# Kernel tuning notes

Measured on AMD Instinct MI355X. Metric: run time of the kernel, lower is better.

## Reference

```python
import jax, jax.numpy as jnp
import numpy as np
import math

B, S, D_MODEL = 8, 1024, 1024
N_INPUT, N_PROCESS = 256, 512
N_HEADS, N_HEADS_IN = 8, 4
HIDDEN = 2 * N_INPUT  # combination_analyzer hidden dim (default n_input*2)
TEMP = 2.0            # router temperature buffer


def _mha(x, w_in, b_in, w_out, b_out, n_heads):
    """torch nn.MultiheadAttention (batch_first, eval mode) self-attention."""
    Bq, Sq, E = x.shape
    qkv = x @ w_in.T + b_in                      # [B,S,3E]
    q, k, v = jnp.split(qkv, 3, axis=-1)
    dh = E // n_heads
    sh = lambda t: t.reshape(Bq, Sq, n_heads, dh).transpose(0, 2, 1, 3)
    q, k, v = sh(q), sh(k), sh(v)
    scores = jnp.einsum('bhqd,bhkd->bhqk', q, k) * (1.0 / math.sqrt(dh))
    attn = jax.nn.softmax(scores, axis=-1)
    out = jnp.einsum('bhqk,bhkd->bhqd', attn, v).transpose(0, 2, 1, 3).reshape(Bq, Sq, E)
    return out @ w_out.T + b_out


def _ln(x, g, b, eps=1e-5):
    m = x.mean(-1, keepdims=True)
    v = ((x - m) ** 2).mean(-1, keepdims=True)
    return (x - m) / jnp.sqrt(v + eps) * g + b


def setup_inputs() -> dict:
    key = jax.random.key(0)
    ks = jax.random.split(key, 24)
    rn = lambda i, shape, s=0.02: jax.random.normal(ks[i], shape, jnp.float32) * s
    return {
        'x': jax.random.normal(ks[0], (B, S, D_MODEL), jnp.float32),
        # DynamicRouter attention (embed=d_model, heads=8)
        'r_in_w': rn(1, (3 * D_MODEL, D_MODEL)), 'r_in_b': jnp.zeros((3 * D_MODEL,), jnp.float32),
        'r_out_w': rn(2, (D_MODEL, D_MODEL)), 'r_out_b': jnp.zeros((D_MODEL,), jnp.float32),
        'aff_w': rn(3, (N_INPUT, D_MODEL)), 'aff_b': jnp.zeros((N_INPUT,), jnp.float32),
        # InputNeurons
        'patterns': rn(4, (N_INPUT, D_MODEL), 0.05),
        'i_in_w': rn(5, (3 * N_INPUT, N_INPUT)), 'i_in_b': jnp.zeros((3 * N_INPUT,), jnp.float32),
        'i_out_w': rn(6, (N_INPUT, N_INPUT)), 'i_out_b': jnp.zeros((N_INPUT,), jnp.float32),
        'ln_g': jnp.ones((N_INPUT,), jnp.float32), 'ln_b': jnp.zeros((N_INPUT,), jnp.float32),
        # ProcessNeurons
        'comb_w': rn(7, (N_PROCESS, N_INPUT), 0.05),
        'out_proj_w': rn(8, (N_PROCESS, D_MODEL), 0.05),
        'a1_w': rn(9, (HIDDEN, N_INPUT)), 'a1_b': jnp.zeros((HIDDEN,), jnp.float32),
        'a2_w': rn(10, (N_PROCESS, HIDDEN)), 'a2_b': jnp.zeros((N_PROCESS,), jnp.float32),
        'k_input': 128, 'k_process': 256,
    }


def reference(x, r_in_w, r_in_b, r_out_w, r_out_b, aff_w, aff_b, patterns,
              i_in_w, i_in_b, i_out_w, i_out_b, ln_g, ln_b,
              comb_w, out_proj_w, a1_w, a1_b, a2_w, a2_b, k_input, k_process):
    Bq = x.shape[0]
    # ---- DynamicRouter (eval mode: no gumbel noise, no score noise) ----
    context = _mha(x, r_in_w, r_in_b, r_out_w, r_out_b, N_HEADS)      # [B,S,D]
    affinity = context @ aff_w.T + aff_b                              # [B,S,N_INPUT]
    scores = affinity.max(axis=1)                                     # [B,N_INPUT]
    logits = scores / TEMP
    soft_w = jax.nn.softmax(logits, axis=-1)
    _, indices = jax.lax.top_k(logits, k_input)                       # [B,k_in]
    mask = jnp.zeros_like(soft_w).at[jnp.arange(Bq)[:, None], indices].set(1.0)
    masked = soft_w * mask
    weights = masked / (masked.sum(-1, keepdims=True) + 1e-8)         # [B,N_INPUT]
    # ---- InputNeurons (eval: dropout off) ----
    acts = jax.nn.gelu(context @ patterns.T, approximate=False)       # [B,S,N_INPUT]
    attn_out = _mha(acts, i_in_w, i_in_b, i_out_w, i_out_b, N_HEADS_IN)
    acts = _ln(acts + attn_out, ln_g, ln_b)
    # ---- Gather routed input neurons, weighted by routing weights ----
    sel_acts = jnp.take_along_axis(acts, indices[:, None, :], axis=2)  # [B,S,k_in]
    sel_w = jnp.take_along_axis(weights, indices, axis=1)              # [B,k_in]
    sel_acts = sel_acts * sel_w[:, None, :]
    # ---- ProcessNeurons ----
    # selected_weights[b,p,j] = comb_w[p, indices[b,j]]
    sel_cw = jnp.take(comb_w, indices, axis=1).transpose(1, 0, 2)      # [B,P,k_in]
    proc_acts = jax.nn.gelu(jnp.einsum('bsk,bpk->bsp', sel_acts, sel_cw), approximate=False)
    input_sel = jnp.zeros((Bq, N_INPUT), jnp.float32).at[jnp.arange(Bq)[:, None], indices].set(1.0)
    relevance = jax.nn.gelu(input_sel @ a1_w.T + a1_b, approximate=False) @ a2_w.T + a2_b  # [B,P]
    act_scores = proc_acts.max(axis=1)                                 # [B,P]
    final_scores = act_scores * jax.nn.sigmoid(relevance)
    _, pidx = jax.lax.top_k(final_scores, k_process)                   # [B,k_p]
    sel_proc = jnp.take_along_axis(proc_acts, pidx[:, None, :], axis=2)  # [B,S,k_p]
    sel_proj = out_proj_w[pidx]                                        # [B,k_p,D]
    out = jnp.einsum('bsk,bkd->bsd', sel_proc, sel_proj)               # [B,S,D]
    # ---- residual (eval: dropout identity) ----
    return x + out
```

## Files before the change

kernel.cpp:

```cpp
#include <hip/hip_runtime.h>
#include <hip/hip_bf16.h>
#include <math.h>

constexpr int NB = 8, NS = 1024, ND = 1024, NIN = 256, NPROC = 512, KIN = 128, KPROC = 256;

typedef __attribute__((ext_vector_type(8))) short bf16x8;
typedef __attribute__((ext_vector_type(4))) float f32x4;

#define VMCNT(n) asm volatile("s_waitcnt vmcnt(" #n ")" ::: "memory")
#define LGKMCNT(n) asm volatile("s_waitcnt lgkmcnt(" #n ")" ::: "memory")

__device__ inline float gelu_f(float x) {
    return 0.5f * x * (1.0f + erff(x * 0.7071067811865476f));
}
__device__ inline unsigned short f2b(float f) {
    __hip_bfloat16 h = __float2bfloat16(f);
    return *reinterpret_cast<unsigned short*>(&h);
}
__device__ inline float b2f(unsigned short u) {
    unsigned int v = (unsigned int)u << 16;
    return __uint_as_float(v);
}
__device__ inline void gload16(const void* g, void* l) {
    __builtin_amdgcn_global_load_lds(
        (const __attribute__((address_space(1))) void*)g,
        (__attribute__((address_space(3))) void*)l, 16, 0, 0);
}

__global__ __launch_bounds__(256)
void cvt_all_kernel(const float* __restrict__ x, const float* __restrict__ rin,
                    const float* __restrict__ rout, const float* __restrict__ affw,
                    const float* __restrict__ patt, const float* __restrict__ iin,
                    const float* __restrict__ iout, const float* __restrict__ aff_b,
                    unsigned short* __restrict__ xb, unsigned short* __restrict__ rinb,
                    unsigned short* __restrict__ routb, unsigned short* __restrict__ affbw,
                    unsigned short* __restrict__ pattb, unsigned short* __restrict__ iinb,
                    unsigned short* __restrict__ ioutb, float* __restrict__ biascat)
{
    if (blockIdx.x == 0) {
        int t = threadIdx.x;
        biascat[t] = aff_b[t];
        biascat[256 + t] = 0.f;
    }
    long gi = (long)blockIdx.x * 256 + threadIdx.x;
    long stride = (long)gridDim.x * 256;
    for (; gi < 3342336; gi += stride) {
        const float4* s; ushort4* d; long off;
        if (gi < 2097152)      { s = (const float4*)x;    d = (ushort4*)xb;    off = gi; }
        else if (gi < 2883584) { s = (const float4*)rin;  d = (ushort4*)rinb;  off = gi - 2097152; }
        else if (gi < 3145728) { s = (const float4*)rout; d = (ushort4*)routb; off = gi - 2883584; }
        else if (gi < 3211264) { s = (const float4*)affw; d = (ushort4*)affbw; off = gi - 3145728; }
        else if (gi < 3276800) { s = (const float4*)patt; d = (ushort4*)pattb; off = gi - 3211264; }
        else if (gi < 3325952) { s = (const float4*)iin;  d = (ushort4*)iinb;  off = gi - 3276800; }
        else                   { s = (const float4*)iout; d = (ushort4*)ioutb; off = gi - 3325952; }
        float4 v = s[off];
        ushort4 o;
        o.x = f2b(v.x); o.y = f2b(v.y); o.z = f2b(v.z); o.w = f2b(v.w);
        d[off] = o;
    }
}

__global__ __launch_bounds__(256)
void gemm128s(const unsigned short* __restrict__ A, int lda,
              const unsigned short* __restrict__ B, int ldb,
              const float* __restrict__ bias,
              unsigned short* __restrict__ C16, int ldc,
              int K, int nbx)
{
    __shared__ __align__(16) unsigned short Ab[3][128 * 32];
    __shared__ __align__(16) unsigned short Bb[3][128 * 32];
    int o = blockIdx.x;
    int cpx = gridDim.x >> 3;
    int swz = (o & 7) * cpx + (o >> 3);
    int by = swz / nbx, bx = swz - by * nbx;
    int row0 = by * 128, col0 = bx * 128;

    int t = threadIdx.x;
    int w = t >> 6, l = t & 63, l15 = l & 15, g = l >> 4;
    int wr = w >> 1, wc = w & 1;
    int NT = K >> 5;

    f32x4 acc[4][4];
#pragma unroll
    for (int i = 0; i < 4; ++i)
#pragma unroll
        for (int j = 0; j < 4; ++j) acc[i][j] = (f32x4){0.f, 0.f, 0.f, 0.f};

    auto STAGE = [&](int c, int kt) {
        int k0 = kt * 32;
#pragma unroll
        for (int i = 0; i < 2; ++i) {
            int gi = t + i * 256;
            int row = gi >> 2, cg = gi & 3;
            int cgs = cg ^ ((row >> 1) & 3);
            gload16(&A[(long)(row0 + row) * lda + k0 + cgs * 8], &Ab[c][gi * 8]);
        }
#pragma unroll
        for (int i = 0; i < 2; ++i) {
            int gi = t + i * 256;
            int row = gi >> 2, cg = gi & 3;
            int cgs = cg ^ ((row >> 1) & 3);
            gload16(&B[(long)(col0 + row) * ldb + k0 + cgs * 8], &Bb[c][gi * 8]);
        }
    };

    STAGE(0, 0);
    STAGE(1, 1);

    int cbr = (g ^ ((l15 >> 1) & 3)) * 16;

    int cur = 0;
    for (int T = 0; T < NT; ++T) {
        if (T + 1 < NT) { VMCNT(4); } else { VMCNT(0); }
        __builtin_amdgcn_s_barrier();
        asm volatile("" ::: "memory");

        const char* Ab_ = (const char*)&Ab[cur][0];
        const char* Bb_ = (const char*)&Bb[cur][0];
        bf16x8 af[4], bfr[4];
#pragma unroll
        for (int mi = 0; mi < 4; ++mi)
            af[mi] = *(const bf16x8*)(Ab_ + (wr * 64 + mi * 16 + l15) * 64 + cbr);
#pragma unroll
        for (int ni = 0; ni < 4; ++ni)
            bfr[ni] = *(const bf16x8*)(Bb_ + (wc * 64 + ni * 16 + l15) * 64 + cbr);

        if (T + 2 < NT) {
            int nxt = cur + 2;
            if (nxt >= 3) nxt -= 3;
            STAGE(nxt, T + 2);
        }

        LGKMCNT(0);
        __builtin_amdgcn_sched_barrier(0);
        __builtin_amdgcn_s_setprio(1);
#pragma unroll
        for (int mi = 0; mi < 4; ++mi)
#pragma unroll
            for (int ni = 0; ni < 4; ++ni)
                acc[mi][ni] = __builtin_amdgcn_mfma_f32_16x16x32_bf16(
                    af[mi], bfr[ni], acc[mi][ni], 0, 0, 0);
        __builtin_amdgcn_s_setprio(0);

        cur = (cur == 2) ? 0 : cur + 1;
    }

#pragma unroll
    for (int mi = 0; mi < 4; ++mi) {
#pragma unroll
        for (int ni = 0; ni < 4; ++ni) {
            int col = col0 + wc * 64 + ni * 16 + l15;
            float bv = bias ? bias[col] : 0.f;
#pragma unroll
            for (int r = 0; r < 4; ++r) {
                int row = row0 + wr * 64 + mi * 16 + g * 4 + r;
                float v = acc[mi][ni][r] + bv;
                float vp = __shfl_xor(v, 1);
                if (!(l15 & 1)) {
                    unsigned int u = (unsigned int)f2b(v) | ((unsigned int)f2b(vp) << 16);
                    *(unsigned int*)&C16[(long)row * ldc + col] = u;
                }
            }
        }
    }
}

__global__ __launch_bounds__(256)
void gemm128x64(const unsigned short* __restrict__ A, int lda,
                const unsigned short* __restrict__ B, int ldb,
                const float* __restrict__ bias,
                unsigned short* __restrict__ C16, int ldc,
                int K, int nbx)
{
    __shared__ __align__(16) unsigned short Ab[3][128 * 32];
    __shared__ __align__(16) unsigned short Bb[3][64 * 32];
    int o = blockIdx.x;
    int cpx = gridDim.x >> 3;
    int swz = (o & 7) * cpx + (o >> 3);
    int by = swz / nbx, bx = swz - by * nbx;
    int row0 = by * 128, col0 = bx * 64;

    int t = threadIdx.x;
    int w = t >> 6, l = t & 63, l15 = l & 15, g = l >> 4;
    int wr = w >> 1, wc = w & 1;
    int NT = K >> 5;

    f32x4 acc[4][2];
#pragma unroll
    for (int i = 0; i < 4; ++i)
#pragma unroll
        for (int j = 0; j < 2; ++j) acc[i][j] = (f32x4){0.f, 0.f, 0.f, 0.f};

    auto STAGE = [&](int c, int kt) {
        int k0 = kt * 32;
#pragma unroll
        for (int i = 0; i < 2; ++i) {
            int gi = t + i * 256;
            int row = gi >> 2, cg = gi & 3;
            int cgs = cg ^ ((row >> 1) & 3);
            gload16(&A[(long)(row0 + row) * lda + k0 + cgs * 8], &Ab[c][gi * 8]);
        }
        {
            int gi = t;
            int row = gi >> 2, cg = gi & 3;
            int cgs = cg ^ ((row >> 1) & 3);
            gload16(&B[(long)(col0 + row) * ldb + k0 + cgs * 8], &Bb[c][gi * 8]);
        }
    };

    STAGE(0, 0);
    STAGE(1, 1);

    int cbr = (g ^ ((l15 >> 1) & 3)) * 16;

    int cur = 0;
    for (int T = 0; T < NT; ++T) {
        if (T + 1 < NT) { VMCNT(3); } else { VMCNT(0); }
        __builtin_amdgcn_s_barrier();
        asm volatile("" ::: "memory");

        const char* Ab_ = (const char*)&Ab[cur][0];
        const char* Bb_ = (const char*)&Bb[cur][0];
        bf16x8 af[4], bfr[2];
#pragma unroll
        for (int mi = 0; mi < 4; ++mi)
            af[mi] = *(const bf16x8*)(Ab_ + (wr * 64 + mi * 16 + l15) * 64 + cbr);
#pragma unroll
        for (int ni = 0; ni < 2; ++ni)
            bfr[ni] = *(const bf16x8*)(Bb_ + (wc * 32 + ni * 16 + l15) * 64 + cbr);

        if (T + 2 < NT) {
            int nxt = cur + 2;
            if (nxt >= 3) nxt -= 3;
            STAGE(nxt, T + 2);
        }

        LGKMCNT(0);
        __builtin_amdgcn_sched_barrier(0);
        __builtin_amdgcn_s_setprio(1);
#pragma unroll
        for (int mi = 0; mi < 4; ++mi)
#pragma unroll
            for (int ni = 0; ni < 2; ++ni)
                acc[mi][ni] = __builtin_amdgcn_mfma_f32_16x16x32_bf16(
                    af[mi], bfr[ni], acc[mi][ni], 0, 0, 0);
        __builtin_amdgcn_s_setprio(0);

        cur = (cur == 2) ? 0 : cur + 1;
    }

#pragma unroll
    for (int mi = 0; mi < 4; ++mi) {
#pragma unroll
        for (int ni = 0; ni < 2; ++ni) {
            int col = col0 + wc * 32 + ni * 16 + l15;
            float bv = bias ? bias[col] : 0.f;
#pragma unroll
            for (int r = 0; r < 4; ++r) {
                int row = row0 + wr * 64 + mi * 16 + g * 4 + r;
                float v = acc[mi][ni][r] + bv;
                float vp = __shfl_xor(v, 1);
                if (!(l15 & 1)) {
                    unsigned int u = (unsigned int)f2b(v) | ((unsigned int)f2b(vp) << 16);
                    *(unsigned int*)&C16[(long)row * ldc + col] = u;
                }
            }
        }
    }
}

__global__ __launch_bounds__(256)
void gemm128e(const unsigned short* __restrict__ A, long sA, int lda,
              const unsigned short* __restrict__ B, long sB, int ldb,
              const float* __restrict__ bias,
              const float* __restrict__ resid, long sR, int ldr,
              float* __restrict__ C32, long sC32, int ldc32,
              unsigned short* __restrict__ C16, long sC16, int ldc16,
              float* __restrict__ C32b, int ldc32b,
              int K, int nbx, int act)
{
    __shared__ __align__(16) unsigned short Ab[3][128 * 32];
    __shared__ __align__(16) unsigned short Bb[3][64 * 32];
    int bz = blockIdx.z;
    const unsigned short* Abase = A + (long)bz * sA;
    const unsigned short* Bbase = B + (long)bz * sB;
    int o = blockIdx.x;
    int cpx = gridDim.x >> 3;
    int swz = (o & 7) * cpx + (o >> 3);
    int by = swz / nbx, bx = swz - by * nbx;
    int row0 = by * 128, col0 = bx * 64;

    int t = threadIdx.x;
    int w = t >> 6, l = t & 63, l15 = l & 15, g = l >> 4;
    int wr = w >> 1, wc = w & 1;
    int NT = K >> 5;

    f32x4 acc[4][2];
#pragma unroll
    for (int i = 0; i < 4; ++i)
#pragma unroll
        for (int j = 0; j < 2; ++j) acc[i][j] = (f32x4){0.f, 0.f, 0.f, 0.f};

    auto STAGE = [&](int c, int kt) {
        int k0 = kt * 32;
#pragma unroll
        for (int i = 0; i < 2; ++i) {
            int gi = t + i * 256;
            int row = gi >> 2, cg = gi & 3;
            int cgs = cg ^ ((row >> 1) & 3);
            gload16(&Abase[(long)(row0 + row) * lda + k0 + cgs * 8], &Ab[c][gi * 8]);
        }
        {
            int gi = t;
            int row = gi >> 2, cg = gi & 3;
            int cgs = cg ^ ((row >> 1) & 3);
            gload16(&Bbase[(long)(col0 + row) * ldb + k0 + cgs * 8], &Bb[c][gi * 8]);
        }
    };

    STAGE(0, 0);
    STAGE(1, 1);

    int cbr = (g ^ ((l15 >> 1) & 3)) * 16;

    int cur = 0;
    for (int T = 0; T < NT; ++T) {
        if (T + 1 < NT) { VMCNT(3); } else { VMCNT(0); }
        __builtin_amdgcn_s_barrier();
        asm volatile("" ::: "memory");

        const char* Ab_ = (const char*)&Ab[cur][0];
        const char* Bb_ = (const char*)&Bb[cur][0];
        bf16x8 af[4], bfr[2];
#pragma unroll
        for (int mi = 0; mi < 4; ++mi)
            af[mi] = *(const bf16x8*)(Ab_ + (wr * 64 + mi * 16 + l15) * 64 + cbr);
#pragma unroll
        for (int ni = 0; ni < 2; ++ni)
            bfr[ni] = *(const bf16x8*)(Bb_ + (wc * 32 + ni * 16 + l15) * 64 + cbr);

        if (T + 2 < NT) {
            int nxt = cur + 2;
            if (nxt >= 3) nxt -= 3;
            STAGE(nxt, T + 2);
        }

        LGKMCNT(0);
        __builtin_amdgcn_sched_barrier(0);
        __builtin_amdgcn_s_setprio(1);
#pragma unroll
        for (int mi = 0; mi < 4; ++mi)
#pragma unroll
            for (int ni = 0; ni < 2; ++ni)
                acc[mi][ni] = __builtin_amdgcn_mfma_f32_16x16x32_bf16(
                    af[mi], bfr[ni], acc[mi][ni], 0, 0, 0);
        __builtin_amdgcn_s_setprio(0);

        cur = (cur == 2) ? 0 : cur + 1;
    }

#pragma unroll
    for (int mi = 0; mi < 4; ++mi) {
#pragma unroll
        for (int ni = 0; ni < 2; ++ni) {
            int col = col0 + wc * 32 + ni * 16 + l15;
            float bv = bias ? bias[col] : 0.f;
#pragma unroll
            for (int r = 0; r < 4; ++r) {
                int row = row0 + wr * 64 + mi * 16 + g * 4 + r;
                float v = acc[mi][ni][r] + bv;
                if (act == 2) {
                    if (col < 256) {
                        C32[(long)row * ldc32 + col] = v;
                    } else {
                        v = gelu_f(v);
                        C32b[(long)row * ldc32b + (col - 256)] = v;
                        C16[(long)row * ldc16 + (col - 256)] = f2b(v);
                    }
                    continue;
                }
                if (act == 1) v = gelu_f(v);
                if (resid) v += resid[(long)bz * sR + (long)row * ldr + col];
                if (C32) C32[(long)bz * sC32 + (long)row * ldc32 + col] = v;
                if (C16) C16[(long)bz * sC16 + (long)row * ldc16 + col] = f2b(v);
            }
        }
    }
}

template <int D>
__global__ __launch_bounds__(256, 2)
void attn_mfma(unsigned short* __restrict__ qkv, int stride, int koff, int voff, float scale)
{
    constexpr int GRL = D / 8;
    constexpr int NITK = (64 * GRL) / 256;
    constexpr int NITV = NITK;
    constexpr int NKS = D / 32;
    constexpr int NF = D / 16;
    constexpr int LV = 72;
    constexpr int LP = 72;
    constexpr int NT = NS / 64;

    __shared__ __align__(16) unsigned short Ks[2][64 * D];
    __shared__ __align__(16) unsigned short Vt[D * LV];
    __shared__ __align__(16) unsigned short Ps[128 * LP];

    int b = blockIdx.z, h = blockIdx.y, qt = blockIdx.x;
    int t = threadIdx.x, w = t >> 6, l = t & 63, l15 = l & 15, g = l >> 4;
    int wq = w * 32;
    long qbase = ((long)b * NS + qt * 128) * stride + h * D;
    long kvbase = (long)b * NS * stride + h * D;

    bf16x8 qreg[2][NKS];
#pragma unroll
    for (int qh = 0; qh < 2; ++qh)
#pragma unroll
        for (int ks = 0; ks < NKS; ++ks)
            qreg[qh][ks] = *(const bf16x8*)&qkv[qbase + (long)(wq + qh * 16 + l15) * stride + g * 8 + ks * 32];

    auto KSTAGE = [&](int c, int kt) {
#pragma unroll
        for (int i = 0; i < NITK; ++i) {
            int gi = t + i * 256;
            int row = gi / GRL, cg = gi % GRL;
            int cgs = cg ^ (row & 7);
            gload16(&qkv[kvbase + (long)(kt * 64 + row) * stride + koff + cgs * 8],
                    &Ks[c][gi * 8]);
        }
    };
    uint4 vp[NITV];
    auto VLOAD = [&](int kt) {
#pragma unroll
        for (int i = 0; i < NITV; ++i) {
            int vgi = t + i * 256;
            int kc = vgi & 63, db = vgi >> 6;
            vp[i] = *(const uint4*)&qkv[kvbase + (long)(kt * 64 + kc) * stride + voff + db * 8];
        }
    };
    auto VWRITE = [&]() {
#pragma unroll
        for (int i = 0; i < NITV; ++i) {
            int vgi = t + i * 256;
            int kc = vgi & 63, db = vgi >> 6;
            uint4 v = vp[i];
            Vt[(db * 8 + 0) * LV + kc] = (unsigned short)(v.x & 0xffff);
            Vt[(db * 8 + 1) * LV + kc] = (unsigned short)(v.x >> 16);
            Vt[(db * 8 + 2) * LV + kc] = (unsigned short)(v.y & 0xffff);
            Vt[(db * 8 + 3) * LV + kc] = (unsigned short)(v.y >> 16);
            Vt[(db * 8 + 4) * LV + kc] = (unsigned short)(v.z & 0xffff);
            Vt[(db * 8 + 5) * LV + kc] = (unsigned short)(v.z >> 16);
            Vt[(db * 8 + 6) * LV + kc] = (unsigned short)(v.w & 0xffff);
            Vt[(db * 8 + 7) * LV + kc] = (unsigned short)(v.w >> 16);
        }
    };

    KSTAGE(0, 0);
    VLOAD(0);
    KSTAGE(1, 1);
    if constexpr (NITK == 4) { VMCNT(4); } else { VMCNT(2); }
    VWRITE();
    LGKMCNT(0);
    __builtin_amdgcn_sched_barrier(0);
    __builtin_amdgcn_s_barrier();

    float m_run[2] = {-INFINITY, -INFINITY};
    float l_run[2] = {0.f, 0.f};
    f32x4 zero4 = {0.f, 0.f, 0.f, 0.f};
    f32x4 oacc[2][NF];
#pragma unroll
    for (int qh = 0; qh < 2; ++qh)
#pragma unroll
        for (int nf = 0; nf < NF; ++nf) oacc[qh][nf] = zero4;

    int xr = (l15 & 7) << 4;
    for (int kt = 0; kt < NT; ++kt) {
        if (kt + 1 < NT) VLOAD(kt + 1);

        const char* ksb = (const char*)&Ks[kt & 1][0];
        f32x4 st[4][2];
#pragma unroll
        for (int f = 0; f < 4; ++f)
#pragma unroll
            for (int qh = 0; qh < 2; ++qh) st[f][qh] = zero4;
#pragma unroll
        for (int ks = 0; ks < NKS; ++ks) {
#pragma unroll
            for (int f = 0; f < 4; ++f) {
                int cb = (g * 16 + ks * 64) ^ xr;
                bf16x8 a = *(const bf16x8*)(ksb + (f * 16 + l15) * (D * 2) + cb);
#pragma unroll
                for (int qh = 0; qh < 2; ++qh)
                    st[f][qh] = __builtin_amdgcn_mfma_f32_16x16x32_bf16(a, qreg[qh][ks], st[f][qh], 0, 0, 0);
            }
        }
#pragma unroll
        for (int qh = 0; qh < 2; ++qh) {
            float pm = -INFINITY;
#pragma unroll
            for (int f = 0; f < 4; ++f) {
                st[f][qh] *= scale;
#pragma unroll
                for (int r = 0; r < 4; ++r) pm = fmaxf(pm, st[f][qh][r]);
            }
            pm = fmaxf(pm, __shfl_xor(pm, 16));
            pm = fmaxf(pm, __shfl_xor(pm, 32));
            float mn = fmaxf(m_run[qh], pm);
            float corr = __expf(m_run[qh] - mn);
            float rs = 0.f;
#pragma unroll
            for (int f = 0; f < 4; ++f) {
                float p0 = __expf(st[f][qh][0] - mn);
                float p1 = __expf(st[f][qh][1] - mn);
                float p2 = __expf(st[f][qh][2] - mn);
                float p3 = __expf(st[f][qh][3] - mn);
                rs += (p0 + p1) + (p2 + p3);
                ushort4 pw;
                pw.x = f2b(p0); pw.y = f2b(p1); pw.z = f2b(p2); pw.w = f2b(p3);
                *(ushort4*)&Ps[(wq + qh * 16 + l15) * LP + f * 16 + g * 4] = pw;
            }
            rs += __shfl_xor(rs, 16);
            rs += __shfl_xor(rs, 32);
            l_run[qh] = l_run[qh] * corr + rs;
            m_run[qh] = mn;
            float corrO[4];
#pragma unroll
            for (int r = 0; r < 4; ++r) corrO[r] = __shfl(corr, g * 4 + r);
#pragma unroll
            for (int nf = 0; nf < NF; ++nf)
#pragma unroll
                for (int r = 0; r < 4; ++r) oacc[qh][nf][r] *= corrO[r];
        }
#pragma unroll
        for (int ks2 = 0; ks2 < 2; ++ks2) {
            bf16x8 vb[NF];
#pragma unroll
            for (int nf = 0; nf < NF; ++nf)
                vb[nf] = *(const bf16x8*)&Vt[(nf * 16 + l15) * LV + ks2 * 32 + g * 8];
#pragma unroll
            for (int qh = 0; qh < 2; ++qh) {
                bf16x8 pa = *(const bf16x8*)&Ps[(wq + qh * 16 + l15) * LP + ks2 * 32 + g * 8];
#pragma unroll
                for (int nf = 0; nf < NF; ++nf)
                    oacc[qh][nf] = __builtin_amdgcn_mfma_f32_16x16x32_bf16(pa, vb[nf], oacc[qh][nf], 0, 0, 0);
            }
        }

        if (kt + 1 < NT) {
            LGKMCNT(0);
            __builtin_amdgcn_sched_barrier(0);
            __builtin_amdgcn_s_barrier();
            if (kt + 2 < NT) {
                KSTAGE(kt & 1, kt + 2);
                if constexpr (NITK == 4) { VMCNT(4); } else { VMCNT(2); }
            } else {
                VMCNT(0);
            }
            VWRITE();
            LGKMCNT(0);
            __builtin_amdgcn_sched_barrier(0);
            __builtin_amdgcn_s_barrier();
        }
    }

#pragma unroll
    for (int qh = 0; qh < 2; ++qh) {
        float lo[4];
#pragma unroll
        for (int r = 0; r < 4; ++r) lo[r] = __shfl(l_run[qh], g * 4 + r);
#pragma unroll
        for (int nf = 0; nf < NF; ++nf)
#pragma unroll
            for (int r = 0; r < 4; ++r) {
                float o = oacc[qh][nf][r] / lo[r];
                qkv[qbase + (long)(wq + qh * 16 + g * 4 + r) * stride + nf * 16 + l15] = f2b(o);
            }
    }
}

__global__ __launch_bounds__(256)
void maxpart_aff_kernel(const float* __restrict__ aff, float* __restrict__ part)
{
    int sc = blockIdx.x, b = blockIdx.y, t = threadIdx.x;
    float m = -INFINITY;
    for (int s = sc * 32; s < (sc + 1) * 32; ++s)
        m = fmaxf(m, aff[((long)b * NS + s) * NIN + t]);
    part[(b * 32 + sc) * NIN + t] = m;
}

__global__ __launch_bounds__(256)
void rank_input_kernel(const float* __restrict__ part, int* __restrict__ idx_out,
                       float* __restrict__ w_out)
{
    int b = blockIdx.x, t = threadIdx.x;
    __shared__ float lg[256], rv[256];
    float m = part[(b * 32) * NIN + t];
#pragma unroll
    for (int sc = 1; sc < 32; ++sc) m = fmaxf(m, part[(b * 32 + sc) * NIN + t]);
    float l = m * 0.5f;
    lg[t] = l;
    rv[t] = l;
    __syncthreads();
    for (int off = 128; off; off >>= 1) {
        if (t < off) rv[t] = fmaxf(rv[t], rv[t + off]);
        __syncthreads();
    }
    float mx = rv[0];
    __syncthreads();
    float e = expf(l - mx);
    rv[t] = e;
    __syncthreads();
    for (int off = 128; off; off >>= 1) {
        if (t < off) rv[t] += rv[t + off];
        __syncthreads();
    }
    float Zs = rv[0];
    float soft = e / Zs;
    __syncthreads();
    int rank = 0;
    for (int j = 0; j < 256; ++j) {
        float vj = lg[j];
        rank += (vj > l) || (vj == l && j < t);
    }
    rv[t] = (rank < KIN) ? soft : 0.f;
    __syncthreads();
    for (int off = 128; off; off >>= 1) {
        if (t < off) rv[t] += rv[t + off];
        __syncthreads();
    }
    float msum = rv[0];
    if (rank < KIN) {
        idx_out[b * KIN + rank] = t;
        w_out[b * KIN + rank] = soft / (msum + 1e-8f);
    }
}

__global__ __launch_bounds__(512)
void rank_proc_kernel(const float* __restrict__ finals, int* __restrict__ pidx)
{
    int b = blockIdx.x, t = threadIdx.x;
    __shared__ float v[512];
    float xv = finals[b * NPROC + t];
    v[t] = xv;
    __syncthreads();
    int rank = 0;
    for (int j = 0; j < 512; ++j) {
        float vj = v[j];
        rank += (vj > xv) || (vj == xv && j < t);
    }
    if (rank < KPROC) pidx[b * KPROC + rank] = t;
}

__global__ __launch_bounds__(256)
void ln_gather_kernel(const float* __restrict__ a, const unsigned short* __restrict__ bsrc,
                      const float* __restrict__ gg, const float* __restrict__ be,
                      const int* __restrict__ idx_in, const float* __restrict__ w_sel,
                      unsigned short* __restrict__ sel_acts)
{
    int w = threadIdx.x >> 6, l = threadIdx.x & 63;
    long row = (long)blockIdx.x * 4 + w;
    int b = (int)(row >> 10);
    __shared__ float lnv[4][256];

    float4 av = *(const float4*)&a[row * 256 + l * 4];
    ushort4 bu = *(const ushort4*)&bsrc[row * 256 + l * 4];
    float v0 = av.x + b2f(bu.x);
    float v1 = av.y + b2f(bu.y);
    float v2 = av.z + b2f(bu.z);
    float v3 = av.w + b2f(bu.w);
    float s = (v0 + v1) + (v2 + v3);
#pragma unroll
    for (int off = 1; off < 64; off <<= 1) s += __shfl_xor(s, off);
    float mean = s * (1.f / 256.f);
    float d0 = v0 - mean, d1 = v1 - mean, d2 = v2 - mean, d3 = v3 - mean;
    float ss = (d0 * d0 + d1 * d1) + (d2 * d2 + d3 * d3);
#pragma unroll
    for (int off = 1; off < 64; off <<= 1) ss += __shfl_xor(ss, off);
    float rstd = rsqrtf(ss * (1.f / 256.f) + 1e-5f);
    float4 gv = *(const float4*)&gg[l * 4];
    float4 bev = *(const float4*)&be[l * 4];
    lnv[w][l * 4 + 0] = d0 * rstd * gv.x + bev.x;
    lnv[w][l * 4 + 1] = d1 * rstd * gv.y + bev.y;
    lnv[w][l * 4 + 2] = d2 * rstd * gv.z + bev.z;
    lnv[w][l * 4 + 3] = d3 * rstd * gv.w + bev.w;
    int id0 = idx_in[b * KIN + l];
    int id1 = idx_in[b * KIN + l + 64];
    sel_acts[row * KIN + l] = f2b(lnv[w][id0] * w_sel[b * KIN + l]);
    sel_acts[row * KIN + l + 64] = f2b(lnv[w][id1] * w_sel[b * KIN + l + 64]);
}

__global__ void gather_sel_cw_b(const float* __restrict__ comb_w, const int* __restrict__ idx_in,
                                unsigned short* __restrict__ sel_cw)
{
    int gidx = blockIdx.x * 256 + threadIdx.x;
    int b = gidx >> 16;
    int rem = gidx & 65535;
    int pb = rem >> 7, j = rem & 127;
    sel_cw[gidx] = f2b(comb_w[pb * NIN + idx_in[b * KIN + j]]);
}

__global__ void gather_sel_proc_b(const unsigned short* __restrict__ proc_acts,
                                  const int* __restrict__ pidx,
                                  unsigned short* __restrict__ sel_proc)
{
    int s = blockIdx.x, b = blockIdx.y, j = threadIdx.x;
    long row = (long)b * NS + s;
    sel_proc[row * KPROC + j] = proc_acts[row * NPROC + pidx[b * KPROC + j]];
}

__global__ void gather_sel_projT(const float* __restrict__ out_proj_w, const int* __restrict__ pidx,
                                 unsigned short* __restrict__ selT)
{
    int gidx = blockIdx.x * 256 + threadIdx.x;
    int b = gidx >> 15;
    int rem = gidx & 32767;
    int d = rem >> 5;
    int kp0 = (rem & 31) * 8;
    unsigned int u[4];
#pragma unroll
    for (int i = 0; i < 4; ++i) {
        unsigned short e0 = f2b(out_proj_w[(long)pidx[b * KPROC + kp0 + 2 * i] * ND + d]);
        unsigned short e1 = f2b(out_proj_w[(long)pidx[b * KPROC + kp0 + 2 * i + 1] * ND + d]);
        u[i] = (unsigned int)e0 | ((unsigned int)e1 << 16);
    }
    uint4 o; o.x = u[0]; o.y = u[1]; o.z = u[2]; o.w = u[3];
    *(uint4*)&selT[((long)b * ND + d) * KPROC + kp0] = o;
}

__global__ __launch_bounds__(512)
void maxpart_kernel(const unsigned short* __restrict__ proc, float* __restrict__ part)
{
    int sc = blockIdx.x, b = blockIdx.y, t = threadIdx.x;
    float m = -INFINITY;
    for (int s = sc * 32; s < (sc + 1) * 32; ++s)
        m = fmaxf(m, b2f(proc[((long)b * NS + s) * NPROC + t]));
    part[(b * 32 + sc) * NPROC + t] = m;
}

__global__ __launch_bounds__(512)
void rel1_kernel(const int* __restrict__ idx_in, const float* __restrict__ a1w,
                 const float* __restrict__ a1b, float* __restrict__ rel1g)
{
    int b = blockIdx.x, t = threadIdx.x;
    __shared__ int sidx[KIN];
    if (t < KIN) sidx[t] = idx_in[b * KIN + t];
    __syncthreads();
    float r1 = a1b[t];
    const float* a1row = a1w + (long)t * NIN;
    for (int j = 0; j < KIN; ++j) r1 += a1row[sidx[j]];
    rel1g[b * 512 + t] = gelu_f(r1);
}

__global__ __launch_bounds__(256)
void finals_kernel(const float* __restrict__ maxpart, const float* __restrict__ rel1g,
                   const float* __restrict__ a2w, const float* __restrict__ a2b,
                   float* __restrict__ finals)
{
    int b = blockIdx.y;
    int w = threadIdx.x >> 6, l = threadIdx.x & 63;
    __shared__ float r1[512];
    for (int i = threadIdx.x; i < 512; i += 256) r1[i] = rel1g[b * 512 + i];
    __syncthreads();
#pragma unroll 1
    for (int pi = 0; pi < 16; ++pi) {
        int p = blockIdx.x * 64 + w * 16 + pi;
        const float* a2row = a2w + (long)p * 512;
        float acc = 0.f;
#pragma unroll
        for (int i = 0; i < 8; ++i)
            acc += a2row[l + i * 64] * r1[l + i * 64];
#pragma unroll
        for (int off = 1; off < 64; off <<= 1) acc += __shfl_xor(acc, off);
        float m = (l < 32) ? maxpart[((long)b * 32 + l) * NPROC + p] : -INFINITY;
#pragma unroll
        for (int off = 1; off < 32; off <<= 1) m = fmaxf(m, __shfl_xor(m, off));
        if (l == 0) {
            float r = acc + a2b[p];
            float sig = 1.f / (1.f + expf(-r));
            finals[b * NPROC + p] = m * sig;
        }
    }
}

extern "C" void kernel_launch(void* const* d_in, const int* in_sizes, int n_in,
                              void* d_out, int out_size, void* d_ws, size_t ws_size,
                              hipStream_t stream)
{
    const float* x       = (const float*)d_in[0];
    const float* r_in_w  = (const float*)d_in[1];
    const float* r_in_b  = (const float*)d_in[2];
    const float* r_out_w = (const float*)d_in[3];
    const float* r_out_b = (const float*)d_in[4];
    const float* aff_w   = (const float*)d_in[5];
    const float* aff_b   = (const float*)d_in[6];
    const float* patterns= (const float*)d_in[7];
    const float* i_in_w  = (const float*)d_in[8];
    const float* i_in_b  = (const float*)d_in[9];
    const float* i_out_w = (const float*)d_in[10];
    const float* i_out_b = (const float*)d_in[11];
    const float* ln_g    = (const float*)d_in[12];
    const float* ln_b    = (const float*)d_in[13];
    const float* comb_w  = (const float*)d_in[14];
    const float* out_proj_w = (const float*)d_in[15];
    const float* a1w     = (const float*)d_in[16];
    const float* a1b     = (const float*)d_in[17];
    const float* a2w     = (const float*)d_in[18];
    const float* a2b     = (const float*)d_in[19];
    float* out = (float*)d_out;

    char* ws = (char*)d_ws;
    unsigned short* qkv1b    = (unsigned short*)(ws + 0);
    unsigned short* contextb = (unsigned short*)(ws + 50331648);
    unsigned short* xb       = (unsigned short*)(ws + 67108864);
    unsigned short* w_rin_b  = (unsigned short*)(ws + 83886080);
    unsigned short* w_rout_b = (unsigned short*)(ws + 90177536);
    unsigned short* w_aff_b  = (unsigned short*)(ws + 92274688);
    unsigned short* patt_b   = (unsigned short*)(ws + 92798976);
    unsigned short* w_iin_b  = (unsigned short*)(ws + 93323264);
    unsigned short* w_iout_b = (unsigned short*)(ws + 93716480);
    float* w_sel   = (float*)(ws + 93855744);
    int*   idx_in  = (int*)(ws + 93859840);
    float* finals  = (float*)(ws + 93863936);
    int*   pidx    = (int*)(ws + 93880320);
    float* affin   = (float*)(ws + 94019584);
    float* acts0   = (float*)(ws + 102408192);
    unsigned short* acts0b = (unsigned short*)(ws + 110796800);
    unsigned short* qkv2b  = (unsigned short*)(ws + 114991104);
    unsigned short* attn2projb = (unsigned short*)(ws + 0);
    unsigned short* proc_actsb = (unsigned short*)(ws + 16777216);
    unsigned short* sel_actsb = (unsigned short*)(ws + 33554432);
    unsigned short* sel_cwb   = (unsigned short*)(ws + 35651584);
    unsigned short* sel_procb = (unsigned short*)(ws + 36700160);
    unsigned short* sel_projT = (unsigned short*)(ws + 40894464);
    float* biascat  = (float*)(ws + 45088768);
    float* part_aff = (float*)(ws + 45091840);
    float* maxpart  = (float*)(ws + 45353984);
    float* rel1g    = (float*)(ws + 45878272);

    cvt_all_kernel<<<2048, 256, 0, stream>>>(
        x, r_in_w, r_out_w, aff_w, patterns, i_in_w, i_out_w, aff_b,
        xb, w_rin_b, w_rout_b, w_aff_b, patt_b, w_iin_b, w_iout_b, biascat);

    gemm128s<<<1536, 256, 0, stream>>>(xb, ND, w_rin_b, ND, r_in_b, qkv1b, 3 * ND, ND, 24);
    attn_mfma<128><<<dim3(8, 8, 8), 256, 0, stream>>>(qkv1b, 3 * ND, ND, 2 * ND, 0.088388347648318447f);
    gemm128x64<<<1024, 256, 0, stream>>>(qkv1b, 3 * ND, w_rout_b, ND, r_out_b, contextb, ND, ND, 16);
    gemm128e<<<dim3(512, 1, 1), 256, 0, stream>>>(
        contextb, 0, ND, w_aff_b, 0, ND, biascat, nullptr, 0, 0,
        affin, 0, NIN, acts0b, 0, NIN, acts0, NIN, ND, 8, 2);
    maxpart_aff_kernel<<<dim3(32, NB), 256, 0, stream>>>(affin, part_aff);
    rank_input_kernel<<<NB, 256, 0, stream>>>(part_aff, idx_in, w_sel);
    gemm128x64<<<768, 256, 0, stream>>>(acts0b, NIN, w_iin_b, NIN, i_in_b, qkv2b, 3 * NIN, NIN, 12);
    attn_mfma<64><<<dim3(8, 4, 8), 256, 0, stream>>>(qkv2b, 3 * NIN, NIN, 2 * NIN, 0.125f);
    gemm128e<<<dim3(256, 1, 1), 256, 0, stream>>>(
        qkv2b, 0, 3 * NIN, w_iout_b, 0, NIN, i_out_b, nullptr, 0, 0,
        nullptr, 0, 0, attn2projb, 0, NIN, nullptr, 0, NIN, 4, 0);
    ln_gather_kernel<<<2048, 256, 0, stream>>>(acts0, attn2projb, ln_g, ln_b,
                                               idx_in, w_sel, sel_actsb);
    gather_sel_cw_b<<<2048, 256, 0, stream>>>(comb_w, idx_in, sel_cwb);
    gemm128e<<<dim3(64, 1, NB), 256, 0, stream>>>(
        sel_actsb, (long)NS * KIN, KIN, sel_cwb, (long)NPROC * KIN, KIN,
        nullptr, nullptr, 0, 0,
        nullptr, 0, 0, proc_actsb, (long)NS * NPROC, NPROC, nullptr, 0, KIN, 8, 1);
    maxpart_kernel<<<dim3(32, NB), 512, 0, stream>>>(proc_actsb, maxpart);
    rel1_kernel<<<NB, 512, 0, stream>>>(idx_in, a1w, a1b, rel1g);
    finals_kernel<<<dim3(8, NB), 256, 0, stream>>>(maxpart, rel1g, a2w, a2b, finals);
    rank_proc_kernel<<<NB, 512, 0, stream>>>(finals, pidx);
    gather_sel_proc_b<<<dim3(NS, NB), KPROC, 0, stream>>>(proc_actsb, pidx, sel_procb);
    gather_sel_projT<<<1024, 256, 0, stream>>>(out_proj_w, pidx, sel_projT);
    gemm128e<<<dim3(128, 1, NB), 256, 0, stream>>>(
        sel_procb, (long)NS * KPROC, KPROC, sel_projT, (long)ND * KPROC, KPROC,
        nullptr, x, (long)NS * ND, ND,
        out, (long)NS * ND, ND, nullptr, 0, 0, nullptr, 0, KPROC, 16, 0);
    (void)in_sizes; (void)n_in; (void)out_size; (void)ws_size;
}
```

Measured before the change: 406.4 us.

## Single-buffer K tile via register staging to raise attention occupancy

The attention kernel's double-buffered K tile in LDS, filled by direct global-to-LDS loads, becomes a single LDS buffer staged through registers, like the V path. The launch-bounds hint goes from 2 to 3 blocks per SIMD. Loads for the next K/V tile now start after the softmax, overlapping only the PV MFMAs instead of the whole iteration. Less LDS per block allows more resident blocks, at the cost of shorter prefetch distance, more VGPR pressure from kp staging, and extra register-to-LDS writes.

New measurement: 516.2 us. 1.27x slower.

```diff
diff --git a/kernel.cpp b/kernel.cpp
--- a/kernel.cpp
+++ b/kernel.cpp
@@ -389,7 +389,7 @@
 }
 
 template <int D>
-__global__ __launch_bounds__(256, 2)
+__global__ __launch_bounds__(256, 3)
 void attn_mfma(unsigned short* __restrict__ qkv, int stride, int koff, int voff, float scale)
 {
     constexpr int GRL = D / 8;
@@ -401,7 +401,7 @@
     constexpr int LP = 72;
     constexpr int NT = NS / 64;
 
-    __shared__ __align__(16) unsigned short Ks[2][64 * D];
+    __shared__ __align__(16) unsigned short Ks[64 * D];
     __shared__ __align__(16) unsigned short Vt[D * LV];
     __shared__ __align__(16) unsigned short Ps[128 * LP];
 
@@ -418,17 +418,24 @@
         for (int ks = 0; ks < NKS; ++ks)
             qreg[qh][ks] = *(const bf16x8*)&qkv[qbase + (long)(wq + qh * 16 + l15) * stride + g * 8 + ks * 32];
 
-    auto KSTAGE = [&](int c, int kt) {
+    uint4 kp[NITK], vp[NITV];
+    auto KLOAD = [&](int kt) {
 #pragma unroll
         for (int i = 0; i < NITK; ++i) {
             int gi = t + i * 256;
             int row = gi / GRL, cg = gi % GRL;
-            int cgs = cg ^ (row & 7);
-            gload16(&qkv[kvbase + (long)(kt * 64 + row) * stride + koff + cgs * 8],
-                    &Ks[c][gi * 8]);
+            kp[i] = *(const uint4*)&qkv[kvbase + (long)(kt * 64 + row) * stride + koff + cg * 8];
         }
     };
-    uint4 vp[NITV];
+    auto KWRITE = [&]() {
+#pragma unroll
+        for (int i = 0; i < NITK; ++i) {
+            int gi = t + i * 256;
+            int row = gi / GRL, cg = gi % GRL;
+            int lg = cg ^ (row & 7);
+            *(uint4*)&Ks[(row * GRL + lg) * 8] = kp[i];
+        }
+    };
     auto VLOAD = [&](int kt) {
 #pragma unroll
         for (int i = 0; i < NITV; ++i) {
@@ -454,10 +461,9 @@
         }
     };
 
-    KSTAGE(0, 0);
+    KLOAD(0);
     VLOAD(0);
-    KSTAGE(1, 1);
-    if constexpr (NITK == 4) { VMCNT(4); } else { VMCNT(2); }
+    KWRITE();
     VWRITE();
     LGKMCNT(0);
     __builtin_amdgcn_sched_barrier(0);
@@ -474,9 +480,7 @@
 
     int xr = (l15 & 7) << 4;
     for (int kt = 0; kt < NT; ++kt) {
-        if (kt + 1 < NT) VLOAD(kt + 1);
-
-        const char* ksb = (const char*)&Ks[kt & 1][0];
+        const char* ksb = (const char*)&Ks[0];
         f32x4 st[4][2];
 #pragma unroll
         for (int f = 0; f < 4; ++f)
@@ -530,6 +534,11 @@
 #pragma unroll
                 for (int r = 0; r < 4; ++r) oacc[qh][nf][r] *= corrO[r];
         }
+        bool pre = (kt + 1 < NT);
+        if (pre) {
+            KLOAD(kt + 1);
+            VLOAD(kt + 1);
+        }
 #pragma unroll
         for (int ks2 = 0; ks2 < 2; ++ks2) {
             bf16x8 vb[NF];
@@ -545,16 +554,11 @@
             }
         }
 
-        if (kt + 1 < NT) {
+        if (pre) {
             LGKMCNT(0);
             __builtin_amdgcn_sched_barrier(0);
             __builtin_amdgcn_s_barrier();
-            if (kt + 2 < NT) {
-                KSTAGE(kt & 1, kt + 2);
-                if constexpr (NITK == 4) { VMCNT(4); } else { VMCNT(2); }
-            } else {
-                VMCNT(0);
-            }
+            KWRITE();
             VWRITE();
             LGKMCNT(0);
             __builtin_amdgcn_sched_barrier(0);
```

## Shrink attention tiles to 64 queries and 32-key blocks for more blocks

Applied to the files above, without the earlier changes.

Reshapes the flash-attention kernel so each block handles 64 query rows (16 per wave) and iterates over 32-key tiles instead of 128 queries and 64 keys. The grid doubles and shared memory per block drops, which is meant to raise occupancy and fill the device better for the 512- and 256-block launches. In exchange, each K/V tile is loaded by twice as many blocks, and the shorter key tiles mean more loop iterations, barriers and softmax rescale steps per unit of work. The occupancy hint in the launch bounds is also dropped.

Measured after the change: 446.6 us. 9.9% more time.

```diff
diff --git a/kernel.cpp b/kernel.cpp
--- a/kernel.cpp
+++ b/kernel.cpp
@@ -389,34 +389,33 @@
 }
 
 template <int D>
-__global__ __launch_bounds__(256, 2)
+__global__ __launch_bounds__(256)
 void attn_mfma(unsigned short* __restrict__ qkv, int stride, int koff, int voff, float scale)
 {
+    constexpr int KVB = 32;
     constexpr int GRL = D / 8;
-    constexpr int NITK = (64 * GRL) / 256;
+    constexpr int NITK = (KVB * GRL) / 256;
     constexpr int NITV = NITK;
     constexpr int NKS = D / 32;
     constexpr int NF = D / 16;
-    constexpr int LV = 72;
-    constexpr int LP = 72;
-    constexpr int NT = NS / 64;
-
-    __shared__ __align__(16) unsigned short Ks[2][64 * D];
+    constexpr int LV = 40;
+    constexpr int LP = 40;
+    constexpr int NT = NS / KVB;
+
+    __shared__ __align__(16) unsigned short Ks[2][KVB * D];
     __shared__ __align__(16) unsigned short Vt[D * LV];
-    __shared__ __align__(16) unsigned short Ps[128 * LP];
+    __shared__ __align__(16) unsigned short Ps[64 * LP];
 
     int b = blockIdx.z, h = blockIdx.y, qt = blockIdx.x;
     int t = threadIdx.x, w = t >> 6, l = t & 63, l15 = l & 15, g = l >> 4;
-    int wq = w * 32;
-    long qbase = ((long)b * NS + qt * 128) * stride + h * D;
+    int wq = w * 16;
+    long qbase = ((long)b * NS + qt * 64) * stride + h * D;
     long kvbase = (long)b * NS * stride + h * D;
 
-    bf16x8 qreg[2][NKS];
-#pragma unroll
-    for (int qh = 0; qh < 2; ++qh)
-#pragma unroll
-        for (int ks = 0; ks < NKS; ++ks)
-            qreg[qh][ks] = *(const bf16x8*)&qkv[qbase + (long)(wq + qh * 16 + l15) * stride + g * 8 + ks * 32];
+    bf16x8 qreg[NKS];
+#pragma unroll
+    for (int ks = 0; ks < NKS; ++ks)
+        qreg[ks] = *(const bf16x8*)&qkv[qbase + (long)(wq + l15) * stride + g * 8 + ks * 32];
 
     auto KSTAGE = [&](int c, int kt) {
 #pragma unroll
@@ -424,7 +423,7 @@
             int gi = t + i * 256;
             int row = gi / GRL, cg = gi % GRL;
             int cgs = cg ^ (row & 7);
-            gload16(&qkv[kvbase + (long)(kt * 64 + row) * stride + koff + cgs * 8],
+            gload16(&qkv[kvbase + (long)(kt * KVB + row) * stride + koff + cgs * 8],
                     &Ks[c][gi * 8]);
         }
     };
@@ -433,15 +432,15 @@
 #pragma unroll
         for (int i = 0; i < NITV; ++i) {
             int vgi = t + i * 256;
-            int kc = vgi & 63, db = vgi >> 6;
-            vp[i] = *(const uint4*)&qkv[kvbase + (long)(kt * 64 + kc) * stride + voff + db * 8];
+            int kc = vgi & (KVB - 1), db = vgi / KVB;
+            vp[i] = *(const uint4*)&qkv[kvbase + (long)(kt * KVB + kc) * stride + voff + db * 8];
         }
     };
     auto VWRITE = [&]() {
 #pragma unroll
         for (int i = 0; i < NITV; ++i) {
             int vgi = t + i * 256;
-            int kc = vgi & 63, db = vgi >> 6;
+            int kc = vgi & (KVB - 1), db = vgi / KVB;
             uint4 v = vp[i];
             Vt[(db * 8 + 0) * LV + kc] = (unsigned short)(v.x & 0xffff);
             Vt[(db * 8 + 1) * LV + kc] = (unsigned short)(v.x >> 16);
@@ -457,92 +456,75 @@
     KSTAGE(0, 0);
     VLOAD(0);
     KSTAGE(1, 1);
-    if constexpr (NITK == 4) { VMCNT(4); } else { VMCNT(2); }
+    if constexpr (NITK == 2) { VMCNT(2); } else { VMCNT(1); }
     VWRITE();
     LGKMCNT(0);
     __builtin_amdgcn_sched_barrier(0);
     __builtin_amdgcn_s_barrier();
 
-    float m_run[2] = {-INFINITY, -INFINITY};
-    float l_run[2] = {0.f, 0.f};
+    float m_run = -INFINITY, l_run = 0.f;
     f32x4 zero4 = {0.f, 0.f, 0.f, 0.f};
-    f32x4 oacc[2][NF];
-#pragma unroll
-    for (int qh = 0; qh < 2; ++qh)
-#pragma unroll
-        for (int nf = 0; nf < NF; ++nf) oacc[qh][nf] = zero4;
+    f32x4 oacc[NF];
+#pragma unroll
+    for (int nf = 0; nf < NF; ++nf) oacc[nf] = zero4;
 
     int xr = (l15 & 7) << 4;
     for (int kt = 0; kt < NT; ++kt) {
         if (kt + 1 < NT) VLOAD(kt + 1);
 
         const char* ksb = (const char*)&Ks[kt & 1][0];
-        f32x4 st[4][2];
-#pragma unroll
-        for (int f = 0; f < 4; ++f)
-#pragma unroll
-            for (int qh = 0; qh < 2; ++qh) st[f][qh] = zero4;
+        f32x4 st[2];
+#pragma unroll
+        for (int f = 0; f < 2; ++f) st[f] = zero4;
 #pragma unroll
         for (int ks = 0; ks < NKS; ++ks) {
 #pragma unroll
-            for (int f = 0; f < 4; ++f) {
+            for (int f = 0; f < 2; ++f) {
                 int cb = (g * 16 + ks * 64) ^ xr;
                 bf16x8 a = *(const bf16x8*)(ksb + (f * 16 + l15) * (D * 2) + cb);
-#pragma unroll
-                for (int qh = 0; qh < 2; ++qh)
-                    st[f][qh] = __builtin_amdgcn_mfma_f32_16x16x32_bf16(a, qreg[qh][ks], st[f][qh], 0, 0, 0);
+                st[f] = __builtin_amdgcn_mfma_f32_16x16x32_bf16(a, qreg[ks], st[f], 0, 0, 0);
             }
         }
-#pragma unroll
-        for (int qh = 0; qh < 2; ++qh) {
-            float pm = -INFINITY;
-#pragma unroll
-            for (int f = 0; f < 4; ++f) {
-                st[f][qh] *= scale;
-#pragma unroll
-                for (int r = 0; r < 4; ++r) pm = fmaxf(pm, st[f][qh][r]);
-            }
-            pm = fmaxf(pm, __shfl_xor(pm, 16));
-            pm = fmaxf(pm, __shfl_xor(pm, 32));
-            float mn = fmaxf(m_run[qh], pm);
-            float corr = __expf(m_run[qh] - mn);
-            float rs = 0.f;
-#pragma unroll
-            for (int f = 0; f < 4; ++f) {
-                float p0 = __expf(st[f][qh][0] - mn);
-                float p1 = __expf(st[f][qh][1] - mn);
-                float p2 = __expf(st[f][qh][2] - mn);
-                float p3 = __expf(st[f][qh][3] - mn);
-                rs += (p0 + p1) + (p2 + p3);
-                ushort4 pw;
-                pw.x = f2b(p0); pw.y = f2b(p1); pw.z = f2b(p2); pw.w = f2b(p3);
-                *(ushort4*)&Ps[(wq + qh * 16 + l15) * LP + f * 16 + g * 4] = pw;
-            }
-            rs += __shfl_xor(rs, 16);
-            rs += __shfl_xor(rs, 32);
-            l_run[qh] = l_run[qh] * corr + rs;
-            m_run[qh] = mn;
-            float corrO[4];
-#pragma unroll
-            for (int r = 0; r < 4; ++r) corrO[r] = __shfl(corr, g * 4 + r);
-#pragma unroll
-            for (int nf = 0; nf < NF; ++nf)
-#pragma unroll
-                for (int r = 0; r < 4; ++r) oacc[qh][nf][r] *= corrO[r];
-        }
-#pragma unroll
-        for (int ks2 = 0; ks2 < 2; ++ks2) {
-            bf16x8 vb[NF];
-#pragma unroll
-            for (int nf = 0; nf < NF; ++nf)
-                vb[nf] = *(const bf16x8*)&Vt[(nf * 16 + l15) * LV + ks2 * 32 + g * 8];
-#pragma unroll
-            for (int qh = 0; qh < 2; ++qh) {
-                bf16x8 pa = *(const bf16x8*)&Ps[(wq + qh * 16 + l15) * LP + ks2 * 32 + g * 8];
-#pragma unroll
-                for (int nf = 0; nf < NF; ++nf)
-                    oacc[qh][nf] = __builtin_amdgcn_mfma_f32_16x16x32_bf16(pa, vb[nf], oacc[qh][nf], 0, 0, 0);
-            }
+        float pm = -INFINITY;
+#pragma unroll
+        for (int f = 0; f < 2; ++f) {
+            st[f] *= scale;
+#pragma unroll
+            for (int r = 0; r < 4; ++r) pm = fmaxf(pm, st[f][r]);
+        }
+        pm = fmaxf(pm, __shfl_xor(pm, 16));
+        pm = fmaxf(pm, __shfl_xor(pm, 32));
+        float mn = fmaxf(m_run, pm);
+        float corr = __expf(m_run - mn);
+        float rs = 0.f;
+#pragma unroll
+        for (int f = 0; f < 2; ++f) {
+            float p0 = __expf(st[f][0] - mn);
+            float p1 = __expf(st[f][1] - mn);
+            float p2 = __expf(st[f][2] - mn);
+            float p3 = __expf(st[f][3] - mn);
+            rs += (p0 + p1) + (p2 + p3);
+            ushort4 pw;
+            pw.x = f2b(p0); pw.y = f2b(p1); pw.z = f2b(p2); pw.w = f2b(p3);
+            *(ushort4*)&Ps[(wq + l15) * LP + f * 16 + g * 4] = pw;
+        }
+        rs += __shfl_xor(rs, 16);
+        rs += __shfl_xor(rs, 32);
+        l_run = l_run * corr + rs;
+        m_run = mn;
+        float corrO[4];
+#pragma unroll
+        for (int r = 0; r < 4; ++r) corrO[r] = __shfl(corr, g * 4 + r);
+#pragma unroll
+        for (int nf = 0; nf < NF; ++nf)
+#pragma unroll
+            for (int r = 0; r < 4; ++r) oacc[nf][r] *= corrO[r];
+
+#pragma unroll
+        for (int nf = 0; nf < NF; ++nf) {
+            bf16x8 vb = *(const bf16x8*)&Vt[(nf * 16 + l15) * LV + g * 8];
+            bf16x8 pa = *(const bf16x8*)&Ps[(wq + l15) * LP + g * 8];
+            oacc[nf] = __builtin_amdgcn_mfma_f32_16x16x32_bf16(pa, vb, oacc[nf], 0, 0, 0);
         }
 
         if (kt + 1 < NT) {
@@ -551,7 +533,7 @@
             __builtin_amdgcn_s_barrier();
             if (kt + 2 < NT) {
                 KSTAGE(kt & 1, kt + 2);
-                if constexpr (NITK == 4) { VMCNT(4); } else { VMCNT(2); }
+                if constexpr (NITK == 2) { VMCNT(2); } else { VMCNT(1); }
             } else {
                 VMCNT(0);
             }
@@ -562,19 +544,16 @@
         }
     }
 
-#pragma unroll
-    for (int qh = 0; qh < 2; ++qh) {
-        float lo[4];
-#pragma unroll
-        for (int r = 0; r < 4; ++r) lo[r] = __shfl(l_run[qh], g * 4 + r);
-#pragma unroll
-        for (int nf = 0; nf < NF; ++nf)
-#pragma unroll
-            for (int r = 0; r < 4; ++r) {
-                float o = oacc[qh][nf][r] / lo[r];
-                qkv[qbase + (long)(wq + qh * 16 + g * 4 + r) * stride + nf * 16 + l15] = f2b(o);
-            }
-    }
+    float lo[4];
+#pragma unroll
+    for (int r = 0; r < 4; ++r) lo[r] = __shfl(l_run, g * 4 + r);
+#pragma unroll
+    for (int nf = 0; nf < NF; ++nf)
+#pragma unroll
+        for (int r = 0; r < 4; ++r) {
+            float o = oacc[nf][r] / lo[r];
+            qkv[qbase + (long)(wq + g * 4 + r) * stride + nf * 16 + l15] = f2b(o);
+        }
 }
 
 __global__ __launch_bounds__(256)
@@ -841,7 +820,7 @@
         xb, w_rin_b, w_rout_b, w_aff_b, patt_b, w_iin_b, w_iout_b, biascat);
 
     gemm128s<<<1536, 256, 0, stream>>>(xb, ND, w_rin_b, ND, r_in_b, qkv1b, 3 * ND, ND, 24);
-    attn_mfma<128><<<dim3(8, 8, 8), 256, 0, stream>>>(qkv1b, 3 * ND, ND, 2 * ND, 0.088388347648318447f);
+    attn_mfma<128><<<dim3(16, 8, 8), 256, 0, stream>>>(qkv1b, 3 * ND, ND, 2 * ND, 0.088388347648318447f);
     gemm128x64<<<1024, 256, 0, stream>>>(qkv1b, 3 * ND, w_rout_b, ND, r_out_b, contextb, ND, ND, 16);
     gemm128e<<<dim3(512, 1, 1), 256, 0, stream>>>(
         contextb, 0, ND, w_aff_b, 0, ND, biascat, nullptr, 0, 0,
@@ -849,7 +828,7 @@
     maxpart_aff_kernel<<<dim3(32, NB), 256, 0, stream>>>(affin, part_aff);
     rank_input_kernel<<<NB, 256, 0, stream>>>(part_aff, idx_in, w_sel);
     gemm128x64<<<768, 256, 0, stream>>>(acts0b, NIN, w_iin_b, NIN, i_in_b, qkv2b, 3 * NIN, NIN, 12);
-    attn_mfma<64><<<dim3(8, 4, 8), 256, 0, stream>>>(qkv2b, 3 * NIN, NIN, 2 * NIN, 0.125f);
+    attn_mfma<64><<<dim3(16, 4, 8), 256, 0, stream>>>(qkv2b, 3 * NIN, NIN, 2 * NIN, 0.125f);
     gemm128e<<<dim3(256, 1, 1), 256, 0, stream>>>(
         qkv2b, 0, 3 * NIN, w_iout_b, 0, NIN, i_out_b, nullptr, 0, 0,
         nullptr, 0, 0, attn2projb, 0, NIN, nullptr, 0, NIN, 4, 0);
```
